# Kernel tuning notes

Measured on AMD Instinct MI355X. Metric: run time of the kernel, lower is better.

## Reference

```python
import jax, jax.numpy as jnp
import numpy as np

N = 20000
E = 320000
IN_F = 256
HEADS = 4
OUT_F = 64
NEG_SLOPE = 0.2


def setup_inputs() -> dict:
    key = jax.random.key(0)
    k1, k2, k3, k4 = jax.random.split(key, 4)
    x = jax.random.normal(k1, (N, IN_F), dtype=jnp.float32)
    edge_index = jax.random.randint(k2, (2, E), 0, N, dtype=jnp.int64)
    # Linear W: [in_features, heads*out_features] (xavier-ish scale)
    W = jax.random.normal(k3, (IN_F, HEADS * OUT_F), dtype=jnp.float32) * (1.0 / np.sqrt(IN_F))
    # attention vector: [1, heads, 2*out_features]
    att = jax.random.normal(k4, (1, HEADS, 2 * OUT_F), dtype=jnp.float32) * 0.1
    b = jnp.zeros((HEADS * OUT_F,), dtype=jnp.float32)
    return {"x": x, "W": W, "att": att, "b": b, "edge_index": edge_index}


def _leaky_relu(v):
    return jnp.where(v > 0, v, NEG_SLOPE * v)


def reference(x, W, att, b, edge_index):
    n = x.shape[0]
    heads = att.shape[1]
    d = att.shape[2] // 2

    # add self loops: edge_index -> [2, E+N]
    loops = jnp.arange(n, dtype=edge_index.dtype)
    src = jnp.concatenate([edge_index[0], loops])
    dst = jnp.concatenate([edge_index[1], loops])

    # projected node features [N, heads, out]
    h = (x @ W).reshape(n, heads, d)

    # attention scores: leaky_relu is elementwise, so the concat-then-dot
    # splits into src/dst halves of `att` -> avoids materializing h_cat.
    a_src = att[0, :, :d]  # [heads, out]
    a_dst = att[0, :, d:]  # [heads, out]
    h_src = h[src]  # [Etot, heads, out]
    scores = (
        jnp.einsum("ehd,hd->eh", _leaky_relu(h_src), a_src)
        + jnp.einsum("ehd,hd->eh", _leaky_relu(h[dst]), a_dst)
    )  # [Etot, heads]

    # NOTE: original module applies softmax over ALL edges (dim=0), not per-dst
    w = jax.nn.softmax(scores, axis=0)  # [Etot, heads]

    # scatter-aggregate weighted src features into dst nodes
    out = jax.ops.segment_sum(h_src * w[:, :, None], dst, num_segments=n)  # [N, heads, out]

    return out.reshape(n, heads * d) + b
```

## Files before the change

kernel.cpp:

```cpp
#include <hip/hip_runtime.h>

#define NN 20000
#define EE 320000
#define TE 340000
#define NEG 0.2f
#define NB_SCORE 1329
#define NB_GEMM 625
#define CAP 96

typedef __attribute__((ext_vector_type(8))) _Float16 half8;
typedef __attribute__((ext_vector_type(4))) _Float16 half4v;
typedef __attribute__((ext_vector_type(4))) float f32x4;

__device__ __forceinline__ float lrelu(float v) { return v > 0.f ? v : NEG * v; }

__global__ __launch_bounds__(256) void k_wsplit(const float* __restrict__ W,
                                                _Float16* __restrict__ Wh, _Float16* __restrict__ Wl) {
    int c = blockIdx.x;
    int k = threadIdx.x;
    float w = W[k * 256 + c];
    _Float16 hi = (_Float16)w;
    _Float16 lo = (_Float16)(w - (float)hi);
    int idx = (k >> 3) * 2048 + c * 8 + (k & 7);
    Wh[idx] = hi;
    Wl[idx] = lo;
}

__global__ __launch_bounds__(256, 4) void k_gemm(const float* __restrict__ x,
                                                 const _Float16* __restrict__ Wh,
                                                 const _Float16* __restrict__ Wl,
                                                 const float* __restrict__ att, _Float16* __restrict__ h16,
                                                 float* __restrict__ Es, float* __restrict__ Ed,
                                                 int* __restrict__ cnt) {
    __shared__ _Float16 xh[32][264];
    __shared__ _Float16 xl[32][264];
    const int tid = threadIdx.x;
    const int r0 = blockIdx.x * 32;

    if (tid < 32) cnt[r0 + tid] = 0;

    const float4* x4 = (const float4*)x;
    #pragma unroll
    for (int i = 0; i < 8; ++i) {
        int slot = tid + i * 256;
        int row = slot >> 6, c4 = slot & 63;
        float4 v = x4[(r0 + row) * 64 + c4];
        _Float16 h0 = (_Float16)v.x, h1 = (_Float16)v.y, h2 = (_Float16)v.z, h3 = (_Float16)v.w;
        half4v hv = {h0, h1, h2, h3};
        half4v lv = {(_Float16)(v.x - (float)h0), (_Float16)(v.y - (float)h1),
                     (_Float16)(v.z - (float)h2), (_Float16)(v.w - (float)h3)};
        *(half4v*)&xh[row][c4 * 4] = hv;
        *(half4v*)&xl[row][c4 * 4] = lv;
    }
    __syncthreads();

    const int lane = tid & 63, wid = tid >> 6;
    const int ch = wid;
    const int grp = lane >> 4, li = lane & 15;

    f32x4 acc[2][4];
    #pragma unroll
    for (int rt = 0; rt < 2; ++rt)
        #pragma unroll
        for (int i = 0; i < 4; ++i) acc[rt][i] = (f32x4){0.f, 0.f, 0.f, 0.f};

    const _Float16* bb_h = Wh + (ch * 64 + li) * 8 + grp * 2048;
    const _Float16* bb_l = Wl + (ch * 64 + li) * 8 + grp * 2048;

    for (int ks = 0; ks < 8; ++ks) {
        half8 ah0 = *(const half8*)&xh[li][ks * 32 + grp * 8];
        half8 al0 = *(const half8*)&xl[li][ks * 32 + grp * 8];
        half8 ah1 = *(const half8*)&xh[16 + li][ks * 32 + grp * 8];
        half8 al1 = *(const half8*)&xl[16 + li][ks * 32 + grp * 8];
        const _Float16* ph = bb_h + ks * 8192;
        const _Float16* pl = bb_l + ks * 8192;
        #pragma unroll
        for (int ct = 0; ct < 4; ++ct) {
            half8 bh = *(const half8*)(ph + ct * 128);
            half8 bl = *(const half8*)(pl + ct * 128);
            acc[0][ct] = __builtin_amdgcn_mfma_f32_16x16x32_f16(ah0, bh, acc[0][ct], 0, 0, 0);
            acc[0][ct] = __builtin_amdgcn_mfma_f32_16x16x32_f16(al0, bh, acc[0][ct], 0, 0, 0);
            acc[0][ct] = __builtin_amdgcn_mfma_f32_16x16x32_f16(ah0, bl, acc[0][ct], 0, 0, 0);
            acc[0][ct] = __builtin_amdgcn_mfma_f32_16x16x32_f16(al0, bl, acc[0][ct], 0, 0, 0);
            acc[1][ct] = __builtin_amdgcn_mfma_f32_16x16x32_f16(ah1, bh, acc[1][ct], 0, 0, 0);
            acc[1][ct] = __builtin_amdgcn_mfma_f32_16x16x32_f16(al1, bh, acc[1][ct], 0, 0, 0);
            acc[1][ct] = __builtin_amdgcn_mfma_f32_16x16x32_f16(ah1, bl, acc[1][ct], 0, 0, 0);
            acc[1][ct] = __builtin_amdgcn_mfma_f32_16x16x32_f16(al1, bl, acc[1][ct], 0, 0, 0);
        }
    }

    float pss[2][4] = {{0.f,0.f,0.f,0.f},{0.f,0.f,0.f,0.f}};
    float psd[2][4] = {{0.f,0.f,0.f,0.f},{0.f,0.f,0.f,0.f}};
    #pragma unroll
    for (int rt = 0; rt < 2; ++rt) {
        #pragma unroll
        for (int ct = 0; ct < 4; ++ct) {
            int cl = ct * 16 + li;
            float avc = att[ch * 128 + cl];
            float dvc = att[ch * 128 + 64 + cl];
            #pragma unroll
            for (int reg = 0; reg < 4; ++reg) {
                float v = acc[rt][ct][reg];
                h16[(r0 + rt * 16 + grp * 4 + reg) * 256 + ch * 64 + cl] = (_Float16)v;
                float l = lrelu(v);
                pss[rt][reg] += l * avc;
                psd[rt][reg] += l * dvc;
            }
        }
    }
    #pragma unroll
    for (int rt = 0; rt < 2; ++rt)
        #pragma unroll
        for (int reg = 0; reg < 4; ++reg) {
            #pragma unroll
            for (int m = 1; m < 16; m <<= 1) {
                pss[rt][reg] += __shfl_xor(pss[rt][reg], m, 64);
                psd[rt][reg] += __shfl_xor(psd[rt][reg], m, 64);
            }
        }
    if (li == 0) {
        #pragma unroll
        for (int rt = 0; rt < 2; ++rt)
            #pragma unroll
            for (int reg = 0; reg < 4; ++reg) {
                int row = r0 + rt * 16 + grp * 4 + reg;
                Es[row * 4 + ch] = expf(pss[rt][reg]);
                Ed[row * 4 + ch] = expf(psd[rt][reg]);
            }
    }
}

__global__ __launch_bounds__(256) void k_fill(const int* __restrict__ es, const int* __restrict__ ed,
                                              const float* __restrict__ Es, const float* __restrict__ Ed,
                                              int* __restrict__ cnt, unsigned short* __restrict__ bucket,
                                              float4* __restrict__ psum) {
    __shared__ float4 ls[4];
    int e = blockIdx.x * 256 + threadIdx.x;
    int tid = threadIdx.x, lane = tid & 63, wid = tid >> 6;
    float4 p = {0.f, 0.f, 0.f, 0.f};
    if (e < TE) {
        int si = e < EE ? es[e] : e - EE;
        int di = e < EE ? ed[e] : e - EE;
        int pos = atomicAdd(cnt + di, 1);
        if (pos < CAP) bucket[di * CAP + pos] = (unsigned short)si;
        float4 a = ((const float4*)Es)[si];
        float4 d = ((const float4*)Ed)[di];
        p.x = a.x * d.x; p.y = a.y * d.y; p.z = a.z * d.z; p.w = a.w * d.w;
    }
    #pragma unroll
    for (int m = 32; m > 0; m >>= 1) {
        p.x += __shfl_xor(p.x, m, 64);
        p.y += __shfl_xor(p.y, m, 64);
        p.z += __shfl_xor(p.z, m, 64);
        p.w += __shfl_xor(p.w, m, 64);
    }
    if (lane == 0) ls[wid] = p;
    __syncthreads();
    if (tid == 0) {
        float4 t;
        t.x = ls[0].x + ls[1].x + ls[2].x + ls[3].x;
        t.y = ls[0].y + ls[1].y + ls[2].y + ls[3].y;
        t.z = ls[0].z + ls[1].z + ls[2].z + ls[3].z;
        t.w = ls[0].w + ls[1].w + ls[2].w + ls[3].w;
        psum[blockIdx.x] = t;
    }
}

__global__ __launch_bounds__(256) void k_comb(const float4* __restrict__ psum, float* __restrict__ hstat) {
    __shared__ float4 zred[4];
    int tid = threadIdx.x, lane = tid & 63, wid = tid >> 6;
    float4 z = {0.f, 0.f, 0.f, 0.f};
    for (int i = tid; i < NB_SCORE; i += 256) {
        float4 s = psum[i];
        z.x += s.x; z.y += s.y; z.z += s.z; z.w += s.w;
    }
    #pragma unroll
    for (int m = 32; m > 0; m >>= 1) {
        z.x += __shfl_xor(z.x, m, 64);
        z.y += __shfl_xor(z.y, m, 64);
        z.z += __shfl_xor(z.z, m, 64);
        z.w += __shfl_xor(z.w, m, 64);
    }
    if (lane == 0) zred[wid] = z;
    __syncthreads();
    if (tid == 0) {
        float4 t;
        t.x = zred[0].x + zred[1].x + zred[2].x + zred[3].x;
        t.y = zred[0].y + zred[1].y + zred[2].y + zred[3].y;
        t.z = zred[0].z + zred[1].z + zred[2].z + zred[3].z;
        t.w = zred[0].w + zred[1].w + zred[2].w + zred[3].w;
        hstat[0] = 1.0f / t.x; hstat[1] = 1.0f / t.y;
        hstat[2] = 1.0f / t.z; hstat[3] = 1.0f / t.w;
    }
}

__global__ __launch_bounds__(256) void k_gather(const int* __restrict__ cnt,
                                                const unsigned short* __restrict__ bucket,
                                                const float* __restrict__ Es, const float* __restrict__ Ed,
                                                const _Float16* __restrict__ h16, const float* __restrict__ b,
                                                const float* __restrict__ hstat, float* __restrict__ out) {
    int n = blockIdx.x * 4 + (threadIdx.x >> 6);
    int lane = threadIdx.x & 63;
    int head = lane >> 4;
    int len = cnt[n]; len = len < CAP ? len : CAP;
    const unsigned short* bsi = bucket + n * CAP;
    const half4v* h4 = (const half4v*)h16;
    float4 a0 = {0.f, 0.f, 0.f, 0.f}, a1 = a0, a2 = a0, a3 = a0;
    int j = 0;
    for (; j + 15 < len; j += 16) {
        int s[16];
        float w[16];
        #pragma unroll
        for (int q = 0; q < 16; ++q) s[q] = bsi[j + q];
        #pragma unroll
        for (int q = 0; q < 16; ++q) w[q] = Es[s[q] * 4 + head];
        half4v v[16];
        #pragma unroll
        for (int q = 0; q < 16; ++q) v[q] = h4[s[q] * 64 + lane];
        #pragma unroll
        for (int q = 0; q < 16; q += 4) {
            a0.x += w[q] * (float)v[q].x;     a0.y += w[q] * (float)v[q].y;
            a0.z += w[q] * (float)v[q].z;     a0.w += w[q] * (float)v[q].w;
            a1.x += w[q+1] * (float)v[q+1].x; a1.y += w[q+1] * (float)v[q+1].y;
            a1.z += w[q+1] * (float)v[q+1].z; a1.w += w[q+1] * (float)v[q+1].w;
            a2.x += w[q+2] * (float)v[q+2].x; a2.y += w[q+2] * (float)v[q+2].y;
            a2.z += w[q+2] * (float)v[q+2].z; a2.w += w[q+2] * (float)v[q+2].w;
            a3.x += w[q+3] * (float)v[q+3].x; a3.y += w[q+3] * (float)v[q+3].y;
            a3.z += w[q+3] * (float)v[q+3].z; a3.w += w[q+3] * (float)v[q+3].w;
        }
    }
    for (; j + 7 < len; j += 8) {
        int s0 = bsi[j],     s1 = bsi[j + 1], s2 = bsi[j + 2], s3 = bsi[j + 3];
        int s4 = bsi[j + 4], s5 = bsi[j + 5], s6 = bsi[j + 6], s7 = bsi[j + 7];
        float w0 = Es[s0 * 4 + head], w1 = Es[s1 * 4 + head];
        float w2 = Es[s2 * 4 + head], w3 = Es[s3 * 4 + head];
        float w4 = Es[s4 * 4 + head], w5 = Es[s5 * 4 + head];
        float w6 = Es[s6 * 4 + head], w7 = Es[s7 * 4 + head];
        half4v v0 = h4[s0 * 64 + lane], v1 = h4[s1 * 64 + lane];
        half4v v2 = h4[s2 * 64 + lane], v3 = h4[s3 * 64 + lane];
        half4v v4 = h4[s4 * 64 + lane], v5 = h4[s5 * 64 + lane];
        half4v v6 = h4[s6 * 64 + lane], v7 = h4[s7 * 64 + lane];
        a0.x += w0 * (float)v0.x; a0.y += w0 * (float)v0.y; a0.z += w0 * (float)v0.z; a0.w += w0 * (float)v0.w;
        a1.x += w1 * (float)v1.x; a1.y += w1 * (float)v1.y; a1.z += w1 * (float)v1.z; a1.w += w1 * (float)v1.w;
        a2.x += w2 * (float)v2.x; a2.y += w2 * (float)v2.y; a2.z += w2 * (float)v2.z; a2.w += w2 * (float)v2.w;
        a3.x += w3 * (float)v3.x; a3.y += w3 * (float)v3.y; a3.z += w3 * (float)v3.z; a3.w += w3 * (float)v3.w;
        a0.x += w4 * (float)v4.x; a0.y += w4 * (float)v4.y; a0.z += w4 * (float)v4.z; a0.w += w4 * (float)v4.w;
        a1.x += w5 * (float)v5.x; a1.y += w5 * (float)v5.y; a1.z += w5 * (float)v5.z; a1.w += w5 * (float)v5.w;
        a2.x += w6 * (float)v6.x; a2.y += w6 * (float)v6.y; a2.z += w6 * (float)v6.z; a2.w += w6 * (float)v6.w;
        a3.x += w7 * (float)v7.x; a3.y += w7 * (float)v7.y; a3.z += w7 * (float)v7.z; a3.w += w7 * (float)v7.w;
    }
    for (; j + 3 < len; j += 4) {
        int s0 = bsi[j], s1 = bsi[j + 1], s2 = bsi[j + 2], s3 = bsi[j + 3];
        float w0 = Es[s0 * 4 + head], w1 = Es[s1 * 4 + head];
        float w2 = Es[s2 * 4 + head], w3 = Es[s3 * 4 + head];
        half4v v0 = h4[s0 * 64 + lane], v1 = h4[s1 * 64 + lane];
        half4v v2 = h4[s2 * 64 + lane], v3 = h4[s3 * 64 + lane];
        a0.x += w0 * (float)v0.x; a0.y += w0 * (float)v0.y; a0.z += w0 * (float)v0.z; a0.w += w0 * (float)v0.w;
        a1.x += w1 * (float)v1.x; a1.y += w1 * (float)v1.y; a1.z += w1 * (float)v1.z; a1.w += w1 * (float)v1.w;
        a2.x += w2 * (float)v2.x; a2.y += w2 * (float)v2.y; a2.z += w2 * (float)v2.z; a2.w += w2 * (float)v2.w;
        a3.x += w3 * (float)v3.x; a3.y += w3 * (float)v3.y; a3.z += w3 * (float)v3.z; a3.w += w3 * (float)v3.w;
    }
    for (; j < len; ++j) {
        int s = bsi[j];
        float w = Es[s * 4 + head];
        half4v hv = h4[s * 64 + lane];
        a0.x += w * (float)hv.x; a0.y += w * (float)hv.y; a0.z += w * (float)hv.z; a0.w += w * (float)hv.w;
    }
    float scale = hstat[head] * Ed[n * 4 + head];
    float4 bb = ((const float4*)b)[lane];
    float4 o;
    o.x = bb.x + scale * (a0.x + a1.x + a2.x + a3.x);
    o.y = bb.y + scale * (a0.y + a1.y + a2.y + a3.y);
    o.z = bb.z + scale * (a0.z + a1.z + a2.z + a3.z);
    o.w = bb.w + scale * (a0.w + a1.w + a2.w + a3.w);
    ((float4*)out)[n * 64 + lane] = o;
}

extern "C" void kernel_launch(void* const* d_in, const int* in_sizes, int n_in,
                              void* d_out, int out_size, void* d_ws, size_t ws_size,
                              hipStream_t stream) {
    const float* x   = (const float*)d_in[0];
    const float* W   = (const float*)d_in[1];
    const float* att = (const float*)d_in[2];
    const float* b   = (const float*)d_in[3];
    const int*  eidx = (const int*)d_in[4];
    const int* es = eidx;
    const int* ed = eidx + EE;
    float* out = (float*)d_out;

    float* ws = (float*)d_ws;
    _Float16* h16 = (_Float16*)ws;
    float* Es     = (float*)(h16 + NN * 256);
    float* Ed     = Es + NN * 4;
    int*   cnt    = (int*)(Ed + NN * 4);
    unsigned short* bucket = (unsigned short*)(cnt + NN);
    float4* psum  = (float4*)(bucket + NN * CAP);
    float* hstat  = (float*)(psum + NB_SCORE + 1);
    _Float16* Wh  = (_Float16*)(hstat + 12);
    _Float16* Wl  = Wh + 256 * 256;

    k_wsplit<<<256, 256, 0, stream>>>(W, Wh, Wl);
    k_gemm  <<<NB_GEMM, 256, 0, stream>>>(x, Wh, Wl, att, h16, Es, Ed, cnt);
    k_fill  <<<NB_SCORE, 256, 0, stream>>>(es, ed, Es, Ed, cnt, bucket, psum);
    k_comb  <<<1, 256, 0, stream>>>(psum, hstat);
    k_gather<<<NN / 4, 256, 0, stream>>>(cnt, bucket, Es, Ed, h16, b, hstat, out);
}
```

Baseline: 84.50 us.

## Fold softmax denominator reduction into gather and drop lo*lo MFMA terms

Removes the single-block k_comb launch: k_fill now uses a fixed 512-block grid-stride loop with accumulated partials, and every k_gather block redundantly reduces those 512 partials into shared memory to get the inverse normaliser. Counter zeroing moves from k_gemm into k_wsplit. The split-fp16 GEMM also drops the lo*lo MFMA products, cutting matrix work by a quarter at a small precision cost. This trades a kernel launch and a tiny kernel for repeated partial-sum reads in each gather block.

```diff
diff --git a/kernel.cpp b/kernel.cpp
--- a/kernel.cpp
+++ b/kernel.cpp
@@ -4,7 +4,7 @@
 #define EE 320000
 #define TE 340000
 #define NEG 0.2f
-#define NB_SCORE 1329
+#define NB_FILL 512
 #define NB_GEMM 625
 #define CAP 96
 
@@ -15,7 +15,10 @@
 __device__ __forceinline__ float lrelu(float v) { return v > 0.f ? v : NEG * v; }
 
 __global__ __launch_bounds__(256) void k_wsplit(const float* __restrict__ W,
-                                                _Float16* __restrict__ Wh, _Float16* __restrict__ Wl) {
+                                                _Float16* __restrict__ Wh, _Float16* __restrict__ Wl,
+                                                int* __restrict__ cnt) {
+    int z = blockIdx.x * 256 + threadIdx.x;
+    if (z < NN) cnt[z] = 0;
     int c = blockIdx.x;
     int k = threadIdx.x;
     float w = W[k * 256 + c];
@@ -30,14 +33,11 @@
                                                  const _Float16* __restrict__ Wh,
                                                  const _Float16* __restrict__ Wl,
                                                  const float* __restrict__ att, _Float16* __restrict__ h16,
-                                                 float* __restrict__ Es, float* __restrict__ Ed,
-                                                 int* __restrict__ cnt) {
+                                                 float* __restrict__ Es, float* __restrict__ Ed) {
     __shared__ _Float16 xh[32][264];
     __shared__ _Float16 xl[32][264];
     const int tid = threadIdx.x;
     const int r0 = blockIdx.x * 32;
-
-    if (tid < 32) cnt[r0 + tid] = 0;
 
     const float4* x4 = (const float4*)x;
     #pragma unroll
@@ -81,11 +81,9 @@
             acc[0][ct] = __builtin_amdgcn_mfma_f32_16x16x32_f16(ah0, bh, acc[0][ct], 0, 0, 0);
             acc[0][ct] = __builtin_amdgcn_mfma_f32_16x16x32_f16(al0, bh, acc[0][ct], 0, 0, 0);
             acc[0][ct] = __builtin_amdgcn_mfma_f32_16x16x32_f16(ah0, bl, acc[0][ct], 0, 0, 0);
-            acc[0][ct] = __builtin_amdgcn_mfma_f32_16x16x32_f16(al0, bl, acc[0][ct], 0, 0, 0);
             acc[1][ct] = __builtin_amdgcn_mfma_f32_16x16x32_f16(ah1, bh, acc[1][ct], 0, 0, 0);
             acc[1][ct] = __builtin_amdgcn_mfma_f32_16x16x32_f16(al1, bh, acc[1][ct], 0, 0, 0);
             acc[1][ct] = __builtin_amdgcn_mfma_f32_16x16x32_f16(ah1, bl, acc[1][ct], 0, 0, 0);
-            acc[1][ct] = __builtin_amdgcn_mfma_f32_16x16x32_f16(al1, bl, acc[1][ct], 0, 0, 0);
         }
     }
 
@@ -135,17 +133,16 @@
                                               int* __restrict__ cnt, unsigned short* __restrict__ bucket,
                                               float4* __restrict__ psum) {
     __shared__ float4 ls[4];
-    int e = blockIdx.x * 256 + threadIdx.x;
     int tid = threadIdx.x, lane = tid & 63, wid = tid >> 6;
     float4 p = {0.f, 0.f, 0.f, 0.f};
-    if (e < TE) {
+    for (int e = blockIdx.x * 256 + tid; e < TE; e += NB_FILL * 256) {
         int si = e < EE ? es[e] : e - EE;
         int di = e < EE ? ed[e] : e - EE;
         int pos = atomicAdd(cnt + di, 1);
         if (pos < CAP) bucket[di * CAP + pos] = (unsigned short)si;
         float4 a = ((const float4*)Es)[si];
         float4 d = ((const float4*)Ed)[di];
-        p.x = a.x * d.x; p.y = a.y * d.y; p.z = a.z * d.z; p.w = a.w * d.w;
+        p.x += a.x * d.x; p.y += a.y * d.y; p.z += a.z * d.z; p.w += a.w * d.w;
     }
     #pragma unroll
     for (int m = 32; m > 0; m >>= 1) {
@@ -166,41 +163,40 @@
     }
 }
 
-__global__ __launch_bounds__(256) void k_comb(const float4* __restrict__ psum, float* __restrict__ hstat) {
-    __shared__ float4 zred[4];
-    int tid = threadIdx.x, lane = tid & 63, wid = tid >> 6;
-    float4 z = {0.f, 0.f, 0.f, 0.f};
-    for (int i = tid; i < NB_SCORE; i += 256) {
-        float4 s = psum[i];
-        z.x += s.x; z.y += s.y; z.z += s.z; z.w += s.w;
-    }
-    #pragma unroll
-    for (int m = 32; m > 0; m >>= 1) {
-        z.x += __shfl_xor(z.x, m, 64);
-        z.y += __shfl_xor(z.y, m, 64);
-        z.z += __shfl_xor(z.z, m, 64);
-        z.w += __shfl_xor(z.w, m, 64);
-    }
-    if (lane == 0) zred[wid] = z;
-    __syncthreads();
-    if (tid == 0) {
-        float4 t;
-        t.x = zred[0].x + zred[1].x + zred[2].x + zred[3].x;
-        t.y = zred[0].y + zred[1].y + zred[2].y + zred[3].y;
-        t.z = zred[0].z + zred[1].z + zred[2].z + zred[3].z;
-        t.w = zred[0].w + zred[1].w + zred[2].w + zred[3].w;
-        hstat[0] = 1.0f / t.x; hstat[1] = 1.0f / t.y;
-        hstat[2] = 1.0f / t.z; hstat[3] = 1.0f / t.w;
-    }
-}
-
 __global__ __launch_bounds__(256) void k_gather(const int* __restrict__ cnt,
                                                 const unsigned short* __restrict__ bucket,
                                                 const float* __restrict__ Es, const float* __restrict__ Ed,
                                                 const _Float16* __restrict__ h16, const float* __restrict__ b,
-                                                const float* __restrict__ hstat, float* __restrict__ out) {
-    int n = blockIdx.x * 4 + (threadIdx.x >> 6);
-    int lane = threadIdx.x & 63;
+                                                const float4* __restrict__ psum, float* __restrict__ out) {
+    __shared__ float4 zred[4];
+    __shared__ float sInvZ[4];
+    int tid = threadIdx.x, lane = tid & 63, wid0 = tid >> 6;
+    {
+        float4 z0 = psum[tid];
+        float4 z1 = psum[tid + 256];
+        float4 z = {z0.x + z1.x, z0.y + z1.y, z0.z + z1.z, z0.w + z1.w};
+        #pragma unroll
+        for (int m = 32; m > 0; m >>= 1) {
+            z.x += __shfl_xor(z.x, m, 64);
+            z.y += __shfl_xor(z.y, m, 64);
+            z.z += __shfl_xor(z.z, m, 64);
+            z.w += __shfl_xor(z.w, m, 64);
+        }
+        if (lane == 0) zred[wid0] = z;
+        __syncthreads();
+        if (tid == 0) {
+            float4 t;
+            t.x = zred[0].x + zred[1].x + zred[2].x + zred[3].x;
+            t.y = zred[0].y + zred[1].y + zred[2].y + zred[3].y;
+            t.z = zred[0].z + zred[1].z + zred[2].z + zred[3].z;
+            t.w = zred[0].w + zred[1].w + zred[2].w + zred[3].w;
+            sInvZ[0] = 1.0f / t.x; sInvZ[1] = 1.0f / t.y;
+            sInvZ[2] = 1.0f / t.z; sInvZ[3] = 1.0f / t.w;
+        }
+        __syncthreads();
+    }
+
+    int n = blockIdx.x * 4 + (tid >> 6);
     int head = lane >> 4;
     int len = cnt[n]; len = len < CAP ? len : CAP;
     const unsigned short* bsi = bucket + n * CAP;
@@ -266,7 +262,7 @@
         half4v hv = h4[s * 64 + lane];
         a0.x += w * (float)hv.x; a0.y += w * (float)hv.y; a0.z += w * (float)hv.z; a0.w += w * (float)hv.w;
     }
-    float scale = hstat[head] * Ed[n * 4 + head];
+    float scale = sInvZ[head] * Ed[n * 4 + head];
     float4 bb = ((const float4*)b)[lane];
     float4 o;
     o.x = bb.x + scale * (a0.x + a1.x + a2.x + a3.x);
@@ -295,13 +291,11 @@
     int*   cnt    = (int*)(Ed + NN * 4);
     unsigned short* bucket = (unsigned short*)(cnt + NN);
     float4* psum  = (float4*)(bucket + NN * CAP);
-    float* hstat  = (float*)(psum + NB_SCORE + 1);
-    _Float16* Wh  = (_Float16*)(hstat + 12);
+    _Float16* Wh  = (_Float16*)(psum + NB_FILL);
     _Float16* Wl  = Wh + 256 * 256;
 
-    k_wsplit<<<256, 256, 0, stream>>>(W, Wh, Wl);
-    k_gemm  <<<NB_GEMM, 256, 0, stream>>>(x, Wh, Wl, att, h16, Es, Ed, cnt);
-    k_fill  <<<NB_SCORE, 256, 0, stream>>>(es, ed, Es, Ed, cnt, bucket, psum);
-    k_comb  <<<1, 256, 0, stream>>>(psum, hstat);
-    k_gather<<<NN / 4, 256, 0, stream>>>(cnt, bucket, Es, Ed, h16, b, hstat, out);
-}
+    k_wsplit<<<256, 256, 0, stream>>>(W, Wh, Wl, cnt);
+    k_gemm  <<<NB_GEMM, 256, 0, stream>>>(x, Wh, Wl, att, h16, Es, Ed);
+    k_fill  <<<NB_FILL, 256, 0, stream>>>(es, ed, Es, Ed, cnt, bucket, psum);
+    k_gather<<<NN / 4, 256, 0, stream>>>(cnt, bucket, Es, Ed, h16, b, psum, out);
+}
```

After: 84.00 us. Within noise of the previous version (-0.6%).
